# Kernel tuning notes

Measured on AMD Instinct MI355X. Metric: run time of the kernel, lower is better.

Reference implementation:

```python
import jax, jax.numpy as jnp
import numpy as np

TAU = 0.07          # contrastive temperature
GAMMA = 2.0         # focal gamma
W_FOCAL = 0.6
W_CONTRASTIVE = 0.2
IGNORE_INDEX = -100
MAX_ANCHORS = 8     # hardcoded cap in ContrastiveLoss
N_NEG_BATCHES = 4   # hardcoded other_batches[:4]


def setup_inputs() -> dict:
    key = jax.random.key(0)
    ks = jax.random.split(key, 5)
    B, M, V = 64, 128, 5003
    S, D = 200, 128
    return {
        "masked_logits": jax.random.normal(ks[0], (B, M, V), dtype=jnp.float32),
        "masked_targets": jax.random.randint(ks[1], (B, M), 0, V, dtype=jnp.int32),
        "masked_mask": jax.random.randint(ks[2], (B, M), 0, 2, dtype=jnp.int32),
        "product_embeddings": jax.random.normal(ks[3], (B, S, D), dtype=jnp.float32),
        "product_ids": jax.random.randint(ks[4], (B, S), 0, V, dtype=jnp.int32),
        "attention_mask": jnp.ones((B, S), dtype=jnp.int32),
    }


def focal_loss(logits, targets, mask):
    # logits [B,M,V] -> flatten to [B*M,V] as in torch
    B, M, V = logits.shape
    logits = logits.reshape(B * M, V)
    targets = targets.reshape(-1)
    mask = mask.reshape(-1)
    valid = (targets != IGNORE_INDEX) & (mask == 1)
    t = jnp.clip(targets, 0, None)
    logp = jax.nn.log_softmax(logits, axis=-1)
    lp = jnp.take_along_axis(logp, t[:, None], axis=1)[:, 0]  # log p_t
    pt = jnp.exp(lp)
    fl = ((1.0 - pt) ** GAMMA) * (-lp) * valid.astype(logits.dtype)
    denom = valid.sum()
    return jnp.where(denom > 0, fl.sum() / denom.astype(logits.dtype), jnp.zeros((), logits.dtype))


def contrastive_loss(emb, pids, amask):
    # emb [B,S,D]
    B, S, D = emb.shape
    norm = jnp.maximum(jnp.linalg.norm(emb, axis=-1, keepdims=True), 1e-12)
    e = emb / norm  # F.normalize
    valid = (amask == 1) & (pids > 0)  # [B,S]
    # first 4 other batch indices per b (static, matches other_batches[:4])
    others = np.stack([np.array([i for i in range(B) if i != b][:N_NEG_BATCHES]) for b in range(B)])  # [B,4]

    def per_b(eb, vb, ne, nv):
        # eb [S,D], vb [S] bool, ne [4,S,D] neighbor embeddings, nv [4,S] their validity
        n = vb.sum()
        n_anch = jnp.minimum(n // 2, MAX_ANCHORS)
        # valid positions first (in order), padded with S
        pos_sorted = jnp.sort(jnp.where(vb, jnp.arange(S), S))
        a_idx = jnp.clip(pos_sorted[:MAX_ANCHORS], 0, S - 1)
        p_idx = jnp.clip(jnp.take(pos_sorted, n_anch + jnp.arange(MAX_ANCHORS), mode="clip"), 0, S - 1)
        sel = jnp.arange(MAX_ANCHORS) < n_anch  # active anchors
        a_e = eb[a_idx]  # [8,D]
        p_e = eb[p_idx]  # [8,D]
        pos_sim = (a_e * p_e).sum(-1) / TAU  # [8]
        negs = ne.reshape(-1, D)             # [4S,D]
        nvm = nv.reshape(-1)                 # [4S]
        neg_sim = (a_e @ negs.T) / TAU       # [8,4S]
        neg_sim = jnp.where(nvm[None, :], neg_sim, -1e9)
        lse = jax.nn.logsumexp(jnp.concatenate([pos_sim[:, None], neg_sim], axis=-1), axis=-1)
        loss_b = jnp.where(sel, lse - pos_sim, 0.0).sum()
        return loss_b, n_anch

    ne = e[others]       # [B,4,S,D]
    nv = valid[others]   # [B,4,S]
    losses, n_anch = jax.vmap(per_b)(e, valid, ne, nv)
    pairs = n_anch.sum()
    return jnp.where(pairs > 0, losses.sum() / pairs.astype(e.dtype), jnp.zeros((), e.dtype))


def reference(masked_logits, masked_targets, masked_mask, product_embeddings, product_ids, attention_mask):
    focal = focal_loss(masked_logits, masked_targets, masked_mask)
    contrastive = contrastive_loss(product_embeddings, product_ids, attention_mask)
    total = W_FOCAL * focal + W_CONTRASTIVE * contrastive
    return total
```

## Files before the change

kernel.cpp:

```cpp
#include <hip/hip_runtime.h>

#define V 5003
#define BB 64
#define SS 200
#define DD 128
#define TAU 0.07f
#define LOG2E 1.4426950408889634f
#define LN2 0.6931471805599453f
#define SHIFT 8.0f

#define WS_CS 16384
#define WS_PR 16448

__global__ __launch_bounds__(256) void fused_loss_kernel(
    const float* __restrict__ logits,
    const int*   __restrict__ targets,
    const int*   __restrict__ mmask,
    const float* __restrict__ emb,
    const int*   __restrict__ pids,
    const int*   __restrict__ amask,
    float* __restrict__ ws)
{
    const int tid  = threadIdx.x;
    const int lane = tid & 63;
    const int wave = tid >> 6;

    __shared__ float wsum[4];
    __shared__ __align__(16) float anchors[8][DD];
    __shared__ float possim[8];
    __shared__ unsigned char validb[SS];
    __shared__ short poslist[16];
    __shared__ int   n_sh;
    __shared__ int   nanch_sh;
    __shared__ float red[4][8];
    __shared__ float contrib_sh[8];

    if (blockIdx.x < 8192) {
        const int r = blockIdx.x;
        const float* row = logits + (size_t)r * V;

        const int tg = targets[r];
        const int mk = mmask[r];
        const int tc = tg < 0 ? 0 : tg;
        const float xt = row[tc];

        const int p = (4 - ((r * 3) & 3)) & 3;
        const int t = 3 - p;
        const float4* row4 = (const float4*)(row + p);
        const float C = -SHIFT * LOG2E;

        float4 v0 = row4[tid];
        float4 v1 = row4[tid + 256];
        float4 v2 = row4[tid + 512];
        float4 v3 = row4[tid + 768];
        const int  i4 = tid + 1024;
        const bool ok = i4 < 1250;
        float4 v4 = row4[ok ? i4 : 0];
        float h = (tid < p) ? row[tid] : -1e30f;
        float u = (tid < t) ? row[p + 5000 + tid] : -1e30f;
        if (!ok) { v4.x = -1e30f; v4.y = -1e30f; v4.z = -1e30f; v4.w = -1e30f; }

        float s0 = exp2f(fmaf(v0.x, LOG2E, C)) + exp2f(fmaf(v1.x, LOG2E, C))
                 + exp2f(fmaf(v2.x, LOG2E, C)) + exp2f(fmaf(v3.x, LOG2E, C))
                 + exp2f(fmaf(v4.x, LOG2E, C));
        float s1 = exp2f(fmaf(v0.y, LOG2E, C)) + exp2f(fmaf(v1.y, LOG2E, C))
                 + exp2f(fmaf(v2.y, LOG2E, C)) + exp2f(fmaf(v3.y, LOG2E, C))
                 + exp2f(fmaf(v4.y, LOG2E, C));
        float s2 = exp2f(fmaf(v0.z, LOG2E, C)) + exp2f(fmaf(v1.z, LOG2E, C))
                 + exp2f(fmaf(v2.z, LOG2E, C)) + exp2f(fmaf(v3.z, LOG2E, C))
                 + exp2f(fmaf(v4.z, LOG2E, C));
        float s3 = exp2f(fmaf(v0.w, LOG2E, C)) + exp2f(fmaf(v1.w, LOG2E, C))
                 + exp2f(fmaf(v2.w, LOG2E, C)) + exp2f(fmaf(v3.w, LOG2E, C))
                 + exp2f(fmaf(v4.w, LOG2E, C));
        s0 += exp2f(fmaf(h, LOG2E, C)) + exp2f(fmaf(u, LOG2E, C));

        float s = (s0 + s1) + (s2 + s3);
        for (int off = 32; off; off >>= 1)
            s += __shfl_xor(s, off, 64);
        if (lane == 0) wsum[wave] = s;
        __syncthreads();

        if (tid == 0) {
            float S = (wsum[0] + wsum[1]) + (wsum[2] + wsum[3]);
            bool valid = (tg != -100) && (mk == 1);
            float lse = SHIFT + log2f(S) * LN2;
            float lp  = xt - lse;
            float pt  = exp2f(lp * LOG2E);
            float om  = 1.0f - pt;
            float fs  = valid ? (om * om * (-lp)) : 0.0f;
            ((float2*)ws)[r] = make_float2(fs, valid ? 1.0f : 0.0f);
        }
    } else {
        const int b = blockIdx.x - 8192;

        if (tid == 0) n_sh = 0;
        __syncthreads();

        if (tid < SS) {
            int idx = b * SS + tid;
            bool v = (amask[idx] == 1) && (pids[idx] > 0);
            validb[tid] = v ? 1 : 0;
            if (v) atomicAdd(&n_sh, 1);
        }
        __syncthreads();

        if (tid == 0) {
            int cnt = 0;
            for (int s = 0; s < SS && cnt < 16; ++s)
                if (validb[s]) poslist[cnt++] = (short)s;
            for (; cnt < 16; ++cnt) poslist[cnt] = (short)(SS - 1);
            int n  = n_sh;
            int na = n / 2;
            if (na > 8) na = 8;
            nanch_sh = na;
        }
        __syncthreads();
        const int n_anch = nanch_sh;

        const float2* embb = (const float2*)(emb + (size_t)b * SS * DD);
        for (int jj = 0; jj < 2; ++jj) {
            int j = wave + jj * 4;
            if (j < n_anch) {
                int ai = poslist[j];
                int pi = poslist[n_anch + j];
                float2 a2 = embb[ai * 64 + lane];
                float2 p2 = embb[pi * 64 + lane];
                float na_ = a2.x * a2.x + a2.y * a2.y;
                float np_ = p2.x * p2.x + p2.y * p2.y;
                float dp  = a2.x * p2.x + a2.y * p2.y;
                for (int off = 32; off; off >>= 1) {
                    na_ += __shfl_xor(na_, off, 64);
                    np_ += __shfl_xor(np_, off, 64);
                    dp  += __shfl_xor(dp,  off, 64);
                }
                float rna = 1.0f / fmaxf(sqrtf(na_), 1e-12f);
                float rnp = 1.0f / fmaxf(sqrtf(np_), 1e-12f);
                anchors[j][2 * lane]     = a2.x * rna;
                anchors[j][2 * lane + 1] = a2.y * rna;
                if (lane == 0) possim[j] = dp * rna * rnp * (1.0f / TAU);
            } else {
                anchors[j][2 * lane]     = 0.0f;
                anchors[j][2 * lane + 1] = 0.0f;
                if (lane == 0) possim[j] = 0.0f;
            }
        }
        __syncthreads();

        float part[8];
        #pragma unroll
        for (int j = 0; j < 8; ++j) part[j] = 0.0f;

        for (int i = 0; i < 4; ++i) {
            int g = tid + i * 256;
            if (g < 4 * SS) {
                int ol = g / SS;
                int s  = g - ol * SS;
                int o  = (ol >= b) ? ol + 1 : ol;
                int idx = o * SS + s;
                if (amask[idx] == 1 && pids[idx] > 0) {
                    const float4* nb = (const float4*)(emb + (size_t)idx * DD);
                    float acc[8];
                    float n2 = 0.0f;
                    #pragma unroll
                    for (int j = 0; j < 8; ++j) acc[j] = 0.0f;
                    #pragma unroll 8
                    for (int c = 0; c < DD / 4; ++c) {
                        float4 x = nb[c];
                        n2 += x.x * x.x + x.y * x.y + x.z * x.z + x.w * x.w;
                        #pragma unroll
                        for (int j = 0; j < 8; ++j) {
                            float4 a = ((const float4*)anchors[j])[c];
                            acc[j] += a.x * x.x + a.y * x.y + a.z * x.z + a.w * x.w;
                        }
                    }
                    float rn = 1.0f / fmaxf(sqrtf(n2), 1e-12f);
                    #pragma unroll
                    for (int j = 0; j < 8; ++j) {
                        float sim = acc[j] * rn * (1.0f / TAU);
                        part[j] += exp2f(sim * LOG2E);
                    }
                }
            }
        }

        #pragma unroll
        for (int j = 0; j < 8; ++j)
            for (int off = 32; off; off >>= 1)
                part[j] += __shfl_xor(part[j], off, 64);
        if (lane == 0) {
            #pragma unroll
            for (int j = 0; j < 8; ++j) red[wave][j] = part[j];
        }
        __syncthreads();

        if (tid < 8) {
            int j = tid;
            float ps = possim[j];
            float S  = exp2f(ps * LOG2E) + red[0][j] + red[1][j] + red[2][j] + red[3][j];
            float lse = log2f(S) * LN2;
            contrib_sh[j] = (j < n_anch) ? (lse - ps) : 0.0f;
        }
        __syncthreads();
        if (tid == 0) {
            float lb = 0.0f;
            for (int j = 0; j < 8; ++j) lb += contrib_sh[j];
            ws[WS_CS + b] = lb;
            ws[WS_PR + b] = (float)n_anch;
        }
    }
}

__global__ __launch_bounds__(1024) void finalize_kernel(
    const float* __restrict__ ws, float* __restrict__ out)
{
    const int tid  = threadIdx.x;
    const int lane = tid & 63;
    const int wave = tid >> 6;
    __shared__ float r_fs[16], r_vc[16], r_cs[16], r_pr[16];

    const float2* f2 = (const float2*)ws;
    float fs = 0.f, vc = 0.f, cs = 0.f, pr = 0.f;
    #pragma unroll
    for (int i = 0; i < 8; ++i) {
        float2 v = f2[tid + i * 1024];
        fs += v.x; vc += v.y;
    }
    if (tid < 64) {
        cs = ws[WS_CS + tid];
        pr = ws[WS_PR + tid];
    }
    for (int off = 32; off; off >>= 1) {
        fs += __shfl_xor(fs, off, 64);
        vc += __shfl_xor(vc, off, 64);
        cs += __shfl_xor(cs, off, 64);
        pr += __shfl_xor(pr, off, 64);
    }
    if (lane == 0) { r_fs[wave] = fs; r_vc[wave] = vc; r_cs[wave] = cs; r_pr[wave] = pr; }
    __syncthreads();
    if (tid == 0) {
        float FS = 0.f, VC = 0.f;
        for (int w = 0; w < 16; ++w) { FS += r_fs[w]; VC += r_vc[w]; }
        float CS = r_cs[0], PR = r_pr[0];
        float focal = VC > 0.0f ? FS / VC : 0.0f;
        float contr = PR > 0.0f ? CS / PR : 0.0f;
        out[0] = 0.6f * focal + 0.2f * contr;
    }
}

extern "C" void kernel_launch(void* const* d_in, const int* in_sizes, int n_in,
                              void* d_out, int out_size, void* d_ws, size_t ws_size,
                              hipStream_t stream) {
    const float* logits  = (const float*)d_in[0];
    const int*   targets = (const int*)d_in[1];
    const int*   mmask   = (const int*)d_in[2];
    const float* emb     = (const float*)d_in[3];
    const int*   pids    = (const int*)d_in[4];
    const int*   amask   = (const int*)d_in[5];
    float* out = (float*)d_out;
    float* ws  = (float*)d_ws;

    hipLaunchKernelGGL(fused_loss_kernel, dim3(8192 + 64), dim3(256), 0, stream,
                       logits, targets, mmask, emb, pids, amask, ws);
    hipLaunchKernelGGL(finalize_kernel, dim3(1), dim3(1024), 0, stream, ws, out);
}
```

Baseline: 281.6 us.

## Process two logit rows per wave with register-pipelined prefetch

```diff
diff --git a/kernel.cpp b/kernel.cpp
--- a/kernel.cpp
+++ b/kernel.cpp
@@ -1,7 +1,6 @@
 #include <hip/hip_runtime.h>
 
 #define V 5003
-#define BB 64
 #define SS 200
 #define DD 128
 #define TAU 0.07f
@@ -11,6 +10,8 @@
 
 #define WS_CS 16384
 #define WS_PR 16448
+
+#define NFB 1024
 
 __global__ __launch_bounds__(256) void fused_loss_kernel(
     const float* __restrict__ logits,
@@ -25,7 +26,6 @@
     const int lane = tid & 63;
     const int wave = tid >> 6;
 
-    __shared__ float wsum[4];
     __shared__ __align__(16) float anchors[8][DD];
     __shared__ float possim[8];
     __shared__ unsigned char validb[SS];
@@ -35,63 +35,95 @@
     __shared__ float red[4][8];
     __shared__ float contrib_sh[8];
 
-    if (blockIdx.x < 8192) {
-        const int r = blockIdx.x;
-        const float* row = logits + (size_t)r * V;
-
-        const int tg = targets[r];
-        const int mk = mmask[r];
-        const int tc = tg < 0 ? 0 : tg;
-        const float xt = row[tc];
-
-        const int p = (4 - ((r * 3) & 3)) & 3;
+    if (blockIdx.x < NFB) {
+        const int W  = blockIdx.x * 4 + wave;
+        const int r0 = W;
+        const int r1 = W + 4096;
+        const float* rowp0 = logits + (size_t)r0 * V;
+        const float* rowp1 = logits + (size_t)r1 * V;
+
+        const int p = (4 - ((r0 * 3) & 3)) & 3;
         const int t = 3 - p;
-        const float4* row4 = (const float4*)(row + p);
+        const float4* b0 = (const float4*)(rowp0 + p);
+        const float4* b1 = (const float4*)(rowp1 + p);
         const float C = -SHIFT * LOG2E;
 
-        float4 v0 = row4[tid];
-        float4 v1 = row4[tid + 256];
-        float4 v2 = row4[tid + 512];
-        float4 v3 = row4[tid + 768];
-        const int  i4 = tid + 1024;
-        const bool ok = i4 < 1250;
-        float4 v4 = row4[ok ? i4 : 0];
-        float h = (tid < p) ? row[tid] : -1e30f;
-        float u = (tid < t) ? row[p + 5000 + tid] : -1e30f;
-        if (!ok) { v4.x = -1e30f; v4.y = -1e30f; v4.z = -1e30f; v4.w = -1e30f; }
-
-        float s0 = exp2f(fmaf(v0.x, LOG2E, C)) + exp2f(fmaf(v1.x, LOG2E, C))
-                 + exp2f(fmaf(v2.x, LOG2E, C)) + exp2f(fmaf(v3.x, LOG2E, C))
-                 + exp2f(fmaf(v4.x, LOG2E, C));
-        float s1 = exp2f(fmaf(v0.y, LOG2E, C)) + exp2f(fmaf(v1.y, LOG2E, C))
-                 + exp2f(fmaf(v2.y, LOG2E, C)) + exp2f(fmaf(v3.y, LOG2E, C))
-                 + exp2f(fmaf(v4.y, LOG2E, C));
-        float s2 = exp2f(fmaf(v0.z, LOG2E, C)) + exp2f(fmaf(v1.z, LOG2E, C))
-                 + exp2f(fmaf(v2.z, LOG2E, C)) + exp2f(fmaf(v3.z, LOG2E, C))
-                 + exp2f(fmaf(v4.z, LOG2E, C));
-        float s3 = exp2f(fmaf(v0.w, LOG2E, C)) + exp2f(fmaf(v1.w, LOG2E, C))
-                 + exp2f(fmaf(v2.w, LOG2E, C)) + exp2f(fmaf(v3.w, LOG2E, C))
-                 + exp2f(fmaf(v4.w, LOG2E, C));
-        s0 += exp2f(fmaf(h, LOG2E, C)) + exp2f(fmaf(u, LOG2E, C));
-
-        float s = (s0 + s1) + (s2 + s3);
-        for (int off = 32; off; off >>= 1)
-            s += __shfl_xor(s, off, 64);
-        if (lane == 0) wsum[wave] = s;
-        __syncthreads();
-
-        if (tid == 0) {
-            float S = (wsum[0] + wsum[1]) + (wsum[2] + wsum[3]);
-            bool valid = (tg != -100) && (mk == 1);
-            float lse = SHIFT + log2f(S) * LN2;
-            float lp  = xt - lse;
-            float pt  = exp2f(lp * LOG2E);
-            float om  = 1.0f - pt;
-            float fs  = valid ? (om * om * (-lp)) : 0.0f;
-            ((float2*)ws)[r] = make_float2(fs, valid ? 1.0f : 0.0f);
+        const int tg0 = targets[r0], tg1 = targets[r1];
+        const int mk0 = mmask[r0],  mk1 = mmask[r1];
+
+        float h0 = (lane < p) ? rowp0[lane] : -1e30f;
+        float u0 = (lane < t) ? rowp0[p + 5000 + lane] : -1e30f;
+        float h1 = (lane < p) ? rowp1[lane] : -1e30f;
+        float u1 = (lane < t) ? rowp1[p + 5000 + lane] : -1e30f;
+
+        float4 buf[4];
+        #pragma unroll
+        for (int k = 0; k < 4; ++k)
+            buf[k] = b0[k * 64 + lane];
+
+        const float xt0 = rowp0[tg0 < 0 ? 0 : tg0];
+        const float xt1 = rowp1[tg1 < 0 ? 0 : tg1];
+
+        const int l19 = (lane < 34) ? lane : 0;
+
+        float sa0=0.f,sa1=0.f,sa2=0.f,sa3=0.f;
+        float sb0=0.f,sb1=0.f,sb2=0.f,sb3=0.f;
+
+        #pragma unroll
+        for (int k = 0; k < 40; ++k) {
+            float4 nxt;
+            if (k + 4 < 40) {
+                const int  kk = k + 4;
+                const bool A  = kk < 20;
+                const int  j  = A ? kk : kk - 20;
+                const float4* base = A ? b0 : b1;
+                const int idx = (j < 19) ? (j * 64 + lane) : (1216 + l19);
+                nxt = base[idx];
+            } else {
+                nxt = make_float4(-1e30f, -1e30f, -1e30f, -1e30f);
+            }
+            float4 x = buf[k & 3];
+            const int j = (k < 20) ? k : k - 20;
+            if (j == 19 && lane >= 34) { x.x = -1e30f; x.y = -1e30f; x.z = -1e30f; x.w = -1e30f; }
+            float e0 = exp2f(fmaf(x.x, LOG2E, C));
+            float e1 = exp2f(fmaf(x.y, LOG2E, C));
+            float e2 = exp2f(fmaf(x.z, LOG2E, C));
+            float e3 = exp2f(fmaf(x.w, LOG2E, C));
+            if (k < 20) { sa0 += e0; sa1 += e1; sa2 += e2; sa3 += e3; }
+            else        { sb0 += e0; sb1 += e1; sb2 += e2; sb3 += e3; }
+            buf[k & 3] = nxt;
+        }
+        sa0 += exp2f(fmaf(h0, LOG2E, C)) + exp2f(fmaf(u0, LOG2E, C));
+        sb0 += exp2f(fmaf(h1, LOG2E, C)) + exp2f(fmaf(u1, LOG2E, C));
+
+        float sA = (sa0 + sa1) + (sa2 + sa3);
+        float sB = (sb0 + sb1) + (sb2 + sb3);
+        for (int off = 32; off; off >>= 1) {
+            sA += __shfl_xor(sA, off, 64);
+            sB += __shfl_xor(sB, off, 64);
+        }
+        if (lane == 0) {
+            {
+                bool valid = (tg0 != -100) && (mk0 == 1);
+                float lse = SHIFT + log2f(sA) * LN2;
+                float lp  = xt0 - lse;
+                float pt  = exp2f(lp * LOG2E);
+                float om  = 1.0f - pt;
+                ((float2*)ws)[r0] = make_float2(valid ? (om * om * (-lp)) : 0.0f,
+                                                valid ? 1.0f : 0.0f);
+            }
+            {
+                bool valid = (tg1 != -100) && (mk1 == 1);
+                float lse = SHIFT + log2f(sB) * LN2;
+                float lp  = xt1 - lse;
+                float pt  = exp2f(lp * LOG2E);
+                float om  = 1.0f - pt;
+                ((float2*)ws)[r1] = make_float2(valid ? (om * om * (-lp)) : 0.0f,
+                                                valid ? 1.0f : 0.0f);
+            }
         }
     } else {
-        const int b = blockIdx.x - 8192;
+        const int b = blockIdx.x - NFB;
 
         if (tid == 0) n_sh = 0;
         __syncthreads();
@@ -259,7 +291,7 @@
     float* out = (float*)d_out;
     float* ws  = (float*)d_ws;
 
-    hipLaunchKernelGGL(fused_loss_kernel, dim3(8192 + 64), dim3(256), 0, stream,
+    hipLaunchKernelGGL(fused_loss_kernel, dim3(NFB + 64), dim3(256), 0, stream,
                        logits, targets, mmask, emb, pids, amask, ws);
     hipLaunchKernelGGL(finalize_kernel, dim3(1), dim3(1024), 0, stream, ws, out);
 }
```

Measured after the change: 278.8 us. Within noise of the previous version (-1.0%).

## Process one logits row per wave with software-pipelined nontemporal loads

Applied to the files above, without the earlier changes.

```diff
diff --git a/kernel.cpp b/kernel.cpp
--- a/kernel.cpp
+++ b/kernel.cpp
@@ -1,7 +1,6 @@
 #include <hip/hip_runtime.h>
 
 #define V 5003
-#define BB 64
 #define SS 200
 #define DD 128
 #define TAU 0.07f
@@ -11,6 +10,17 @@
 
 #define WS_CS 16384
 #define WS_PR 16448
+
+#define NFB 2048
+
+typedef float f4 __attribute__((ext_vector_type(4)));
+
+__device__ __forceinline__ f4 ldnt4(const f4* p) {
+    return __builtin_nontemporal_load(p);
+}
+__device__ __forceinline__ float ldnt1(const float* p) {
+    return __builtin_nontemporal_load(p);
+}
 
 __global__ __launch_bounds__(256) void fused_loss_kernel(
     const float* __restrict__ logits,
@@ -25,7 +35,6 @@
     const int lane = tid & 63;
     const int wave = tid >> 6;
 
-    __shared__ float wsum[4];
     __shared__ __align__(16) float anchors[8][DD];
     __shared__ float possim[8];
     __shared__ unsigned char validb[SS];
@@ -35,63 +44,67 @@
     __shared__ float red[4][8];
     __shared__ float contrib_sh[8];
 
-    if (blockIdx.x < 8192) {
-        const int r = blockIdx.x;
-        const float* row = logits + (size_t)r * V;
+    if (blockIdx.x < NFB) {
+        const int r = blockIdx.x * 4 + wave;
+        const float* rowp = logits + (size_t)r * V;
+
+        const int p = (4 - ((r * 3) & 3)) & 3;
+        const int t = 3 - p;
+        const f4* b0 = (const f4*)(rowp + p);
+        const float C = -SHIFT * LOG2E;
 
         const int tg = targets[r];
         const int mk = mmask[r];
-        const int tc = tg < 0 ? 0 : tg;
-        const float xt = row[tc];
-
-        const int p = (4 - ((r * 3) & 3)) & 3;
-        const int t = 3 - p;
-        const float4* row4 = (const float4*)(row + p);
-        const float C = -SHIFT * LOG2E;
-
-        float4 v0 = row4[tid];
-        float4 v1 = row4[tid + 256];
-        float4 v2 = row4[tid + 512];
-        float4 v3 = row4[tid + 768];
-        const int  i4 = tid + 1024;
-        const bool ok = i4 < 1250;
-        float4 v4 = row4[ok ? i4 : 0];
-        float h = (tid < p) ? row[tid] : -1e30f;
-        float u = (tid < t) ? row[p + 5000 + tid] : -1e30f;
-        if (!ok) { v4.x = -1e30f; v4.y = -1e30f; v4.z = -1e30f; v4.w = -1e30f; }
-
-        float s0 = exp2f(fmaf(v0.x, LOG2E, C)) + exp2f(fmaf(v1.x, LOG2E, C))
-                 + exp2f(fmaf(v2.x, LOG2E, C)) + exp2f(fmaf(v3.x, LOG2E, C))
-                 + exp2f(fmaf(v4.x, LOG2E, C));
-        float s1 = exp2f(fmaf(v0.y, LOG2E, C)) + exp2f(fmaf(v1.y, LOG2E, C))
-                 + exp2f(fmaf(v2.y, LOG2E, C)) + exp2f(fmaf(v3.y, LOG2E, C))
-                 + exp2f(fmaf(v4.y, LOG2E, C));
-        float s2 = exp2f(fmaf(v0.z, LOG2E, C)) + exp2f(fmaf(v1.z, LOG2E, C))
-                 + exp2f(fmaf(v2.z, LOG2E, C)) + exp2f(fmaf(v3.z, LOG2E, C))
-                 + exp2f(fmaf(v4.z, LOG2E, C));
-        float s3 = exp2f(fmaf(v0.w, LOG2E, C)) + exp2f(fmaf(v1.w, LOG2E, C))
-                 + exp2f(fmaf(v2.w, LOG2E, C)) + exp2f(fmaf(v3.w, LOG2E, C))
-                 + exp2f(fmaf(v4.w, LOG2E, C));
+
+        float h = (lane < p) ? ldnt1(rowp + lane) : -1e30f;
+        float u = (lane < t) ? ldnt1(rowp + p + 5000 + lane) : -1e30f;
+
+        f4 buf[4];
+        #pragma unroll
+        for (int k = 0; k < 4; ++k)
+            buf[k] = ldnt4(b0 + k * 64 + lane);
+
+        const float xt = rowp[tg < 0 ? 0 : tg];
+
+        const int l19 = (lane < 34) ? lane : 0;
+
+        float s0 = 0.f, s1 = 0.f, s2 = 0.f, s3 = 0.f;
+
+        #pragma unroll
+        for (int k = 0; k < 20; ++k) {
+            f4 nxt;
+            if (k + 4 < 20) {
+                const int kk  = k + 4;
+                const int idx = (kk < 19) ? (kk * 64 + lane) : (1216 + l19);
+                nxt = ldnt4(b0 + idx);
+            } else {
+                nxt = (f4)(-1e30f);
+            }
+            f4 x = buf[k & 3];
+            if (k == 19 && lane >= 34) x = (f4)(-1e30f);
+            s0 += exp2f(fmaf(x.x, LOG2E, C));
+            s1 += exp2f(fmaf(x.y, LOG2E, C));
+            s2 += exp2f(fmaf(x.z, LOG2E, C));
+            s3 += exp2f(fmaf(x.w, LOG2E, C));
+            buf[k & 3] = nxt;
+        }
         s0 += exp2f(fmaf(h, LOG2E, C)) + exp2f(fmaf(u, LOG2E, C));
 
         float s = (s0 + s1) + (s2 + s3);
         for (int off = 32; off; off >>= 1)
             s += __shfl_xor(s, off, 64);
-        if (lane == 0) wsum[wave] = s;
-        __syncthreads();
-
-        if (tid == 0) {
-            float S = (wsum[0] + wsum[1]) + (wsum[2] + wsum[3]);
+
+        if (lane == 0) {
             bool valid = (tg != -100) && (mk == 1);
-            float lse = SHIFT + log2f(S) * LN2;
+            float lse = SHIFT + log2f(s) * LN2;
             float lp  = xt - lse;
             float pt  = exp2f(lp * LOG2E);
             float om  = 1.0f - pt;
-            float fs  = valid ? (om * om * (-lp)) : 0.0f;
-            ((float2*)ws)[r] = make_float2(fs, valid ? 1.0f : 0.0f);
+            ((float2*)ws)[r] = make_float2(valid ? (om * om * (-lp)) : 0.0f,
+                                           valid ? 1.0f : 0.0f);
         }
     } else {
-        const int b = blockIdx.x - 8192;
+        const int b = blockIdx.x - NFB;
 
         if (tid == 0) n_sh = 0;
         __syncthreads();
@@ -259,7 +272,7 @@
     float* out = (float*)d_out;
     float* ws  = (float*)d_ws;
 
-    hipLaunchKernelGGL(fused_loss_kernel, dim3(8192 + 64), dim3(256), 0, stream,
+    hipLaunchKernelGGL(fused_loss_kernel, dim3(NFB + 64), dim3(256), 0, stream,
                        logits, targets, mmask, emb, pids, amask, ws);
     hipLaunchKernelGGL(finalize_kernel, dim3(1), dim3(1024), 0, stream, ws, out);
 }
```

Result: faster. 269.5 us (-4.3%).
